# Performance work log

Measured on AMD Instinct MI355X. Metric: run time of the kernel, lower is better.

The kernel has to match this reference:

```python
import jax, jax.numpy as jnp
import numpy as np

D_IN = 1024
D_OUT = 1024

def setup_inputs() -> dict:
    key = jax.random.key(0)
    k1, k2 = jax.random.split(key)
    x = jax.random.normal(k1, (4, 2048, D_IN), dtype=jnp.float32)
    # Keras 'uniform' initializer: U(-0.05, 0.05); kernel has 4 slices, only 0..2 used
    kernel = jax.random.uniform(k2, (4, D_IN, D_OUT), dtype=jnp.float32, minval=-0.05, maxval=0.05)
    return {"x": x, "kernel": kernel}

def reference(x, kernel):
    # QKV projections: x [b, s, d] @ kernel[i] [d, e]
    WQ = jnp.einsum('bsd,de->bse', x, kernel[0])
    WK = jnp.einsum('bsd,de->bse', x, kernel[1])
    WV = jnp.einsum('bsd,de->bse', x, kernel[2])
    scale = 1.0 / jnp.sqrt(jnp.asarray(D_OUT, dtype=WQ.dtype))
    QK = jnp.einsum('bqe,bke->bqk', WQ, WK) * scale  # [b, s, s]
    A = jax.nn.softmax(QK, axis=-1)
    return jnp.einsum('bqk,bke->bqe', A, WV)  # [b, s, e]
```

## Files before the change

kernel.cpp:

```cpp
#include <hip/hip_runtime.h>
#include <hip/hip_bf16.h>
#include <cstdio>

typedef __bf16  bf16x8 __attribute__((ext_vector_type(8)));
typedef float   f32x4  __attribute__((ext_vector_type(4)));
typedef unsigned short u16;
typedef u16     u16x8  __attribute__((ext_vector_type(8)));
typedef u16     u16x4  __attribute__((ext_vector_type(4)));


__device__ __forceinline__ void gld_lds16(const void* g, void* l) {
  __builtin_amdgcn_global_load_lds(
      (const __attribute__((address_space(1))) unsigned int*)g,
      (__attribute__((address_space(3))) unsigned int*)l,
      16, 0, 0);
}

__device__ __forceinline__ u16 f2bf(float f) {
  union { float f; unsigned int u; } c{f};
  unsigned int u = c.u;
  u += 0x7fffu + ((u >> 16) & 1u);
  return (u16)(u >> 16);
}

__device__ __forceinline__ float bf2f(u16 h) {
  union { unsigned int u; float f; } c{(unsigned int)h << 16};
  return c.f;
}

enum { EPI_QKV = 0, EPI_QK = 1, EPI_PV = 2, EPI_VT = 3 };


__global__ __launch_bounds__(256) void prep_kernel(const float* __restrict__ x,
                                                   u16* __restrict__ xbf,
                                                   const float* __restrict__ w,
                                                   u16* __restrict__ wt,
                                                   float* __restrict__ rs) {
  __shared__ float tile[32][33];
  const int bid = blockIdx.x;
  if (bid < 4096) {
    const int i = (bid * 256 + threadIdx.x) * 8;
    float4 a = *(const float4*)(x + i);
    float4 b = *(const float4*)(x + i + 4);
    u16x8 r;
    r[0] = f2bf(a.x); r[1] = f2bf(a.y); r[2] = f2bf(a.z); r[3] = f2bf(a.w);
    r[4] = f2bf(b.x); r[5] = f2bf(b.y); r[6] = f2bf(b.z); r[7] = f2bf(b.w);
    *(u16x8*)(xbf + i) = r;
  } else if (bid < 7168) {
    const int b2 = bid - 4096;
    const int s = b2 >> 10, r = b2 & 1023;
    const int e0 = (r & 31) * 32, d0 = (r >> 5) * 32;
    const int tx = threadIdx.x & 31, ty = threadIdx.x >> 5;
    const float* in = w + (size_t)s * 1048576;
#pragma unroll
    for (int j = 0; j < 4; ++j)
      tile[ty + j * 8][tx] = in[(size_t)(d0 + ty + j * 8) * 1024 + e0 + tx];
    __syncthreads();
    u16* o = wt + (size_t)s * 1048576;
#pragma unroll
    for (int j = 0; j < 4; ++j)
      o[(size_t)(e0 + ty + j * 8) * 1024 + d0 + tx] = f2bf(tile[tx][ty + j * 8]);
  } else {
    const float4 z = {0.f, 0.f, 0.f, 0.f};
#pragma unroll
    for (int j = 0; j < 8; ++j)
      ((float4*)rs)[threadIdx.x + j * 256] = z;
  }
}


template <int GX, int GY, int GZ>
__device__ __forceinline__ void xcd_swz(int& bx, int& by, int& bz) {
  constexpr int NWG = GX * GY * GZ;
  static_assert(NWG % 8 == 0, "grid must be divisible by 8");
  constexpr int Q8 = NWG / 8;
  int flat = blockIdx.x + GX * (blockIdx.y + GY * blockIdx.z);
  flat = (flat & 7) * Q8 + (flat >> 3);
  bx = flat % GX;
  by = (flat / GX) % GY;
  bz = flat / (GX * GY);
}


__device__ __forceinline__ void stage_half(const u16* __restrict__ g, int ld, int k0,
                                           u16* ldsb, int w, int l) {
  const int srow = l >> 3;
  const int scol = ((l & 7) ^ (srow & 7)) * 8;
#pragma unroll
  for (int q = 0; q < 2; ++q) {
    const int r = w * 16 + q * 8;
    gld_lds16(g + (long)(r + srow) * ld + k0 + scol, (void*)(ldsb + r * 64));
  }
}

template <int EPI, int GX, int GY, int GZ>
__global__ __launch_bounds__(512, 2)
void gemm256_bt(const u16* __restrict__ A, const u16* __restrict__ B,
                void* __restrict__ Cv, int K, int lda, int ldb, int ldc,
                long sA, long sB, long sC,
                float* __restrict__ rowsum, u16* __restrict__ auxK, u16* __restrict__ auxV) {
  __shared__ __align__(16) u16 lds[65536];

  const int t = threadIdx.x;
  const int w = t >> 6, l = t & 63;
  const int wm = w >> 2, wn = w & 3;
  const int lr = l & 15, lq = l >> 4;
  const int rsw = l & 7;
  int bxs, bys, bz;
  xcd_swz<GX, GY, GZ>(bxs, bys, bz);
  const int m0 = bys * 256, n0 = bxs * 256;
  const u16* Ar = A + (long)bz * sA + (long)m0 * lda;
  const u16* Br = B + (long)bz * sB + (long)n0 * ldb;

  u16* curA = lds;
  u16* curB = lds + 16384;
  u16* nxtA = lds + 32768;
  u16* nxtB = lds + 49152;

  const int nt = K >> 6;

  f32x4 acc[8][4] = {};

  stage_half(Ar,             lda, 0, curA,        w, l);
  stage_half(Br,             ldb, 0, curB,        w, l);
  stage_half(Br + 128 * ldb, ldb, 0, curB + 8192, w, l);
  stage_half(Ar + 128 * lda, lda, 0, curA + 8192, w, l);
  asm volatile("s_waitcnt vmcnt(4)" ::: "memory");
  if (nt > 1) {
    stage_half(Ar,             lda, 64, nxtA,        w, l);
    stage_half(Br,             ldb, 64, nxtB,        w, l);
    stage_half(Br + 128 * ldb, ldb, 64, nxtB + 8192, w, l);
    asm volatile("s_waitcnt vmcnt(6)" ::: "memory");
  } else {
    asm volatile("s_waitcnt vmcnt(0)" ::: "memory");
  }
  __builtin_amdgcn_s_barrier();

  for (int tt = 0; tt < nt; ++tt) {
    const int kc = tt << 6;
    bf16x8 a0[4][2], a1[4][2], b0[2][2], b1[2][2];

#pragma unroll
    for (int mi = 0; mi < 4; ++mi)
#pragma unroll
      for (int j = 0; j < 2; ++j)
        a0[mi][j] = *(const bf16x8*)(curA + (wm * 128 + mi * 16 + lr) * 64 +
                                     (((j * 4 + lq) ^ rsw) * 8));
#pragma unroll
    for (int ni = 0; ni < 2; ++ni)
#pragma unroll
      for (int j = 0; j < 2; ++j)
        b0[ni][j] = *(const bf16x8*)(curB + (wn * 64 + ni * 16 + lr) * 64 +
                                     (((j * 4 + lq) ^ rsw) * 8));
    if (tt + 1 < nt)
      stage_half(Ar + 128 * lda, lda, kc + 64, nxtA + 8192, w, l);
    __builtin_amdgcn_s_barrier();
    asm volatile("s_waitcnt lgkmcnt(0)" ::: "memory");
    __builtin_amdgcn_sched_barrier(0);
    __builtin_amdgcn_s_setprio(1);
#pragma unroll
    for (int mi = 0; mi < 4; ++mi)
#pragma unroll
      for (int ni = 0; ni < 2; ++ni)
#pragma unroll
        for (int j = 0; j < 2; ++j)
          acc[mi][ni] = __builtin_amdgcn_mfma_f32_16x16x32_bf16(a0[mi][j], b0[ni][j], acc[mi][ni], 0, 0, 0);
    __builtin_amdgcn_s_setprio(0);
    __builtin_amdgcn_s_barrier();

#pragma unroll
    for (int ni = 0; ni < 2; ++ni)
#pragma unroll
      for (int j = 0; j < 2; ++j)
        b1[ni][j] = *(const bf16x8*)(curB + (wn * 64 + (ni + 2) * 16 + lr) * 64 +
                                     (((j * 4 + lq) ^ rsw) * 8));
    __builtin_amdgcn_s_barrier();
    asm volatile("s_waitcnt lgkmcnt(0)" ::: "memory");
    __builtin_amdgcn_sched_barrier(0);
    __builtin_amdgcn_s_setprio(1);
#pragma unroll
    for (int mi = 0; mi < 4; ++mi)
#pragma unroll
      for (int ni = 0; ni < 2; ++ni)
#pragma unroll
        for (int j = 0; j < 2; ++j)
          acc[mi][ni + 2] = __builtin_amdgcn_mfma_f32_16x16x32_bf16(a0[mi][j], b1[ni][j], acc[mi][ni + 2], 0, 0, 0);
    __builtin_amdgcn_s_setprio(0);
    __builtin_amdgcn_s_barrier();

#pragma unroll
    for (int mi = 0; mi < 4; ++mi)
#pragma unroll
      for (int j = 0; j < 2; ++j)
        a1[mi][j] = *(const bf16x8*)(curA + (wm * 128 + (mi + 4) * 16 + lr) * 64 +
                                     (((j * 4 + lq) ^ rsw) * 8));
    if (tt + 2 < nt)
      stage_half(Br, ldb, kc + 128, curB, w, l);
    __builtin_amdgcn_s_barrier();
    asm volatile("s_waitcnt lgkmcnt(0)" ::: "memory");
    __builtin_amdgcn_sched_barrier(0);
    __builtin_amdgcn_s_setprio(1);
#pragma unroll
    for (int mi = 0; mi < 4; ++mi)
#pragma unroll
      for (int ni = 0; ni < 2; ++ni)
#pragma unroll
        for (int j = 0; j < 2; ++j)
          acc[mi + 4][ni + 2] = __builtin_amdgcn_mfma_f32_16x16x32_bf16(a1[mi][j], b1[ni][j], acc[mi + 4][ni + 2], 0, 0, 0);
    __builtin_amdgcn_s_setprio(0);
    __builtin_amdgcn_s_barrier();

    if (tt + 2 < nt) {
      stage_half(Br + 128 * ldb, ldb, kc + 128, curB + 8192, w, l);
      stage_half(Ar,             lda, kc + 128, curA,        w, l);
    }
    __builtin_amdgcn_s_barrier();
    __builtin_amdgcn_sched_barrier(0);
    __builtin_amdgcn_s_setprio(1);
#pragma unroll
    for (int mi = 0; mi < 4; ++mi)
#pragma unroll
      for (int ni = 0; ni < 2; ++ni)
#pragma unroll
        for (int j = 0; j < 2; ++j)
          acc[mi + 4][ni] = __builtin_amdgcn_mfma_f32_16x16x32_bf16(a1[mi][j], b0[ni][j], acc[mi + 4][ni], 0, 0, 0);
    __builtin_amdgcn_s_setprio(0);
    if (tt + 2 < nt)      asm volatile("s_waitcnt vmcnt(6)" ::: "memory");
    else if (tt + 1 < nt) asm volatile("s_waitcnt vmcnt(0)" ::: "memory");
    __builtin_amdgcn_s_barrier();

    { u16* x_ = curA; curA = nxtA; nxtA = x_; }
    { u16* y_ = curB; curB = nxtB; nxtB = y_; }
  }

  if (EPI == EPI_QK) {
#pragma unroll
    for (int mi = 0; mi < 8; ++mi) {
#pragma unroll
      for (int i = 0; i < 4; ++i) {
        const int row = m0 + wm * 128 + mi * 16 + lq * 4 + i;
        float rs = 0.f;
#pragma unroll
        for (int ni = 0; ni < 4; ++ni) {
          const int col = n0 + wn * 64 + ni * 16 + lr;
          const u16 h = f2bf(__expf(acc[mi][ni][i] * 0.03125f));
          ((u16*)Cv)[(long)bz * sC + (long)row * ldc + col] = h;
          rs += bf2f(h);
        }
        rs += __shfl_xor(rs, 1, 64);
        rs += __shfl_xor(rs, 2, 64);
        rs += __shfl_xor(rs, 4, 64);
        rs += __shfl_xor(rs, 8, 64);
        if (lr == 0) atomicAdd(rowsum + bz * 2048 + row, rs);
      }
    }
    return;
  }

  u16* qkv_out = (n0 < 1024) ? (u16*)Cv : auxK;
  const int nl0 = n0 & 1023;
#pragma unroll
  for (int mi = 0; mi < 8; ++mi) {
#pragma unroll
    for (int i = 0; i < 4; ++i) {
      const int row = m0 + wm * 128 + mi * 16 + lq * 4 + i;
#pragma unroll
      for (int ni = 0; ni < 4; ++ni)
        qkv_out[(long)row * 1024 + nl0 + wn * 64 + ni * 16 + lr] = f2bf(acc[mi][ni][i]);
    }
  }
}


template <int EPI, int GX, int GY, int GZ>
__global__ __launch_bounds__(256)
void gemm_bt(const u16* __restrict__ A, const u16* __restrict__ B,
             void* __restrict__ Cv, int K, int lda, int ldb, int ldc,
             long sA, long sB, long sC,
             float* __restrict__ rowsum, u16* __restrict__ auxK, u16* __restrict__ auxV) {
  __shared__ __align__(16) u16 lds[128 * 128];
  u16* As = lds;
  u16* Bs = lds + 128 * 64;

  const int t = threadIdx.x;
  const int w = t >> 6, l = t & 63;
  int bxs, bys, bz;
  xcd_swz<GX, GY, GZ>(bxs, bys, bz);
  const u16* Ab = A + (long)bz * sA;
  const u16* Bb = B + (long)bz * sB;
  const int m0 = bys * 128, n0 = bxs * 128;
  const int wm = w & 1, wn = w >> 1;
  const int lr = l & 15, lq = l >> 4;
  const int srow = l >> 3;
  const int scol = ((l & 7) ^ ((l >> 3) & 7)) * 8;
  const int rsw = l & 7;

  f32x4 acc[4][4] = {};

  for (int k0 = 0; k0 < K; k0 += 64) {
    __syncthreads();
#pragma unroll
    for (int c = 0; c < 4; ++c) {
      const int rb = (w * 4 + c) * 8;
      gld_lds16(Ab + (long)(m0 + rb + srow) * lda + k0 + scol, (void*)(As + rb * 64));
      gld_lds16(Bb + (long)(n0 + rb + srow) * ldb + k0 + scol, (void*)(Bs + rb * 64));
    }
    __syncthreads();
#pragma unroll
    for (int j = 0; j < 2; ++j) {
      bf16x8 af[4], bfr[4];
#pragma unroll
      for (int i = 0; i < 4; ++i) {
        const int ch = ((j * 4 + lq) ^ rsw) * 8;
        af[i]  = *(const bf16x8*)(As + (wm * 64 + i * 16 + lr) * 64 + ch);
        bfr[i] = *(const bf16x8*)(Bs + (wn * 64 + i * 16 + lr) * 64 + ch);
      }
#pragma unroll
      for (int mi = 0; mi < 4; ++mi)
#pragma unroll
        for (int ni = 0; ni < 4; ++ni)
          acc[mi][ni] = __builtin_amdgcn_mfma_f32_16x16x32_bf16(af[mi], bfr[ni], acc[mi][ni], 0, 0, 0);
    }
  }

#pragma unroll
  for (int mi = 0; mi < 4; ++mi) {
#pragma unroll
    for (int i = 0; i < 4; ++i) {
      const int row = m0 + wm * 64 + mi * 16 + lq * 4 + i;
      float inv;
      if (EPI == EPI_PV) inv = 1.0f / rowsum[bz * 2048 + row];
      float rs = 0.f;
#pragma unroll
      for (int ni = 0; ni < 4; ++ni) {
        const float val = acc[mi][ni][i];
        const int col = n0 + wn * 64 + ni * 16 + lr;
        if (EPI == EPI_VT) {
          auxV[(long)(col >> 11) * 2097152 + (long)row * 2048 + (col & 2047)] = f2bf(val);
        } else if (EPI == EPI_QK) {
          const u16 h = f2bf(__expf(val * 0.03125f));
          ((u16*)Cv)[(long)bz * sC + (long)row * ldc + col] = h;
          rs += bf2f(h);
        } else {
          ((float*)Cv)[(long)bz * sC + (long)row * ldc + col] = val * inv;
        }
      }
      if (EPI == EPI_QK) {
        rs += __shfl_xor(rs, 1, 64);
        rs += __shfl_xor(rs, 2, 64);
        rs += __shfl_xor(rs, 4, 64);
        rs += __shfl_xor(rs, 8, 64);
        if (lr == 0) atomicAdd(rowsum + bz * 2048 + row, rs);
      }
    }
  }
}


extern "C" void kernel_launch(void* const* d_in, const int* in_sizes, int n_in,
                              void* d_out, int out_size, void* d_ws, size_t ws_size,
                              hipStream_t stream) {
  (void)in_sizes; (void)n_in; (void)out_size;
  const float* x    = (const float*)d_in[0];
  const float* kern = (const float*)d_in[1];
  float* out = (float*)d_out;
  char* ws = (char*)d_ws;
  const size_t MB = 1024 * 1024;
  u16*   xbf  = (u16*)(ws);
  u16*   WT   = (u16*)(ws + 16 * MB);
  u16*   Qc   = (u16*)(ws + 22 * MB);
  u16*   Kc   = (u16*)(ws + 38 * MB);
  u16*   VT   = (u16*)(ws + 54 * MB);
  u16*   SP   = (u16*)(ws + 70 * MB);
  float* RS   = (float*)(ws + 102 * MB);
  if (ws_size < 102 * MB + 32768)
    fprintf(stderr, "WARNING: ws_size %zu too small\n", ws_size);

  prep_kernel<<<7169, 256, 0, stream>>>(x, xbf, kern, WT, RS);
  gemm256_bt<EPI_QKV, 8, 32, 1><<<dim3(8, 32, 1), 512, 0, stream>>>(
      xbf, WT, Qc, 1024, 1024, 1024, 1024, 0, 0, 0, nullptr, Kc, nullptr);
  gemm_bt<EPI_VT, 64, 8, 1><<<dim3(64, 8, 1), 256, 0, stream>>>(
      WT + 2 * 1048576, xbf, nullptr, 1024, 1024, 1024, 2048,
      0, 0, 0, nullptr, nullptr, VT);
  gemm256_bt<EPI_QK, 8, 8, 4><<<dim3(8, 8, 4), 512, 0, stream>>>(
      Qc, Kc, SP, 1024, 1024, 1024, 2048,
      2048L * 1024, 2048L * 1024, 2048L * 2048, RS, nullptr, nullptr);
  gemm_bt<EPI_PV, 8, 16, 4><<<dim3(8, 16, 4), 256, 0, stream>>>(
      SP, VT, out, 2048, 2048, 2048, 1024,
      2048L * 2048, 1024L * 2048, 2048L * 1024, RS, nullptr, nullptr);
}
```

Before: 242.9 us.

## Restructure GEMM main loop into two-phase ping-pong with register-prefetched B fragments

Replaces the four-phase per-tile schedule, which had many barriers, with a two-phase schedule. The loop is unrolled by two over ping-pong LDS buffers via a macro. The next tile's A and B fragments are loaded into alternating register sets (bE/bO) while the current tile's MFMAs run, and the LDS buffer is refilled one tile ahead, cutting barriers per tile from eight to two. This trades more live VGPRs (two full B fragment sets) and coarser synchronization for less barrier stall. It assumes an even tile count, since the second macro call runs for tt+1 without a bound check.

```diff
diff --git a/kernel.cpp b/kernel.cpp
--- a/kernel.cpp
+++ b/kernel.cpp
@@ -93,6 +93,75 @@
   }
 }
 
+#define KT2(CA, CB, NA, NB, BC0, BC1, BN0, BN1, TT)                               \
+  do {                                                                            \
+           \
+    if ((TT) + 2 < nt) {                                                          \
+      stage_half(Br,             ldb, ((TT) + 2) << 6, lds + (CB),        w, l);  \
+      stage_half(Br + 128 * ldb, ldb, ((TT) + 2) << 6, lds + (CB) + 8192, w, l);  \
+    }                                                                             \
+    _Pragma("unroll")                                                             \
+    for (int mi = 0; mi < 4; ++mi)                                                \
+      _Pragma("unroll")                                                           \
+      for (int j = 0; j < 2; ++j)                                                 \
+        a1[mi][j] = *(const bf16x8*)(lds + (CA) +                                 \
+            (wm * 128 + (mi + 4) * 16 + lr) * 64 + (((j * 4 + lq) ^ rsw) * 8));   \
+    __builtin_amdgcn_s_setprio(1);                                                \
+    _Pragma("unroll")                                                             \
+    for (int mi = 0; mi < 4; ++mi)                                                \
+      _Pragma("unroll")                                                           \
+      for (int ni = 0; ni < 2; ++ni)                                              \
+        _Pragma("unroll")                                                         \
+        for (int j = 0; j < 2; ++j) {                                             \
+          acc[mi][ni]     = __builtin_amdgcn_mfma_f32_16x16x32_bf16(              \
+              a0[mi][j], BC0[ni][j], acc[mi][ni], 0, 0, 0);                       \
+          acc[mi][ni + 2] = __builtin_amdgcn_mfma_f32_16x16x32_bf16(              \
+              a0[mi][j], BC1[ni][j], acc[mi][ni + 2], 0, 0, 0);                   \
+        }                                                                         \
+    __builtin_amdgcn_s_setprio(0);                                                \
+    asm volatile("s_waitcnt lgkmcnt(0)" ::: "memory");                            \
+    if ((TT) + 2 < nt) asm volatile("s_waitcnt vmcnt(4)" ::: "memory");           \
+    else               asm volatile("s_waitcnt vmcnt(0)" ::: "memory");           \
+    __builtin_amdgcn_s_barrier();                                                 \
+         \
+    if ((TT) + 2 < nt) {                                                          \
+      stage_half(Ar,             lda, ((TT) + 2) << 6, lds + (CA),        w, l);  \
+      stage_half(Ar + 128 * lda, lda, ((TT) + 2) << 6, lds + (CA) + 8192, w, l);  \
+    }                                                                             \
+    if ((TT) + 1 < nt) {                                                          \
+      _Pragma("unroll")                                                           \
+      for (int mi = 0; mi < 4; ++mi)                                              \
+        _Pragma("unroll")                                                         \
+        for (int j = 0; j < 2; ++j)                                               \
+          a0[mi][j] = *(const bf16x8*)(lds + (NA) +                               \
+              (wm * 128 + mi * 16 + lr) * 64 + (((j * 4 + lq) ^ rsw) * 8));       \
+      _Pragma("unroll")                                                           \
+      for (int ni = 0; ni < 2; ++ni)                                              \
+        _Pragma("unroll")                                                         \
+        for (int j = 0; j < 2; ++j) {                                             \
+          BN0[ni][j] = *(const bf16x8*)(lds + (NB) +                              \
+              (wn * 64 + ni * 16 + lr) * 64 + (((j * 4 + lq) ^ rsw) * 8));        \
+          BN1[ni][j] = *(const bf16x8*)(lds + (NB) +                              \
+              (wn * 64 + (ni + 2) * 16 + lr) * 64 + (((j * 4 + lq) ^ rsw) * 8));  \
+        }                                                                         \
+    }                                                                             \
+    __builtin_amdgcn_s_setprio(1);                                                \
+    _Pragma("unroll")                                                             \
+    for (int mi = 0; mi < 4; ++mi)                                                \
+      _Pragma("unroll")                                                           \
+      for (int ni = 0; ni < 2; ++ni)                                              \
+        _Pragma("unroll")                                                         \
+        for (int j = 0; j < 2; ++j) {                                             \
+          acc[mi + 4][ni + 2] = __builtin_amdgcn_mfma_f32_16x16x32_bf16(          \
+              a1[mi][j], BC1[ni][j], acc[mi + 4][ni + 2], 0, 0, 0);               \
+          acc[mi + 4][ni]     = __builtin_amdgcn_mfma_f32_16x16x32_bf16(          \
+              a1[mi][j], BC0[ni][j], acc[mi + 4][ni], 0, 0, 0);                   \
+        }                                                                         \
+    __builtin_amdgcn_s_setprio(0);                                                \
+    asm volatile("s_waitcnt lgkmcnt(0)" ::: "memory");                            \
+    __builtin_amdgcn_s_barrier();                                                 \
+  } while (0)
+
 template <int EPI, int GX, int GY, int GZ>
 __global__ __launch_bounds__(512, 2)
 void gemm256_bt(const u16* __restrict__ A, const u16* __restrict__ B,
@@ -112,125 +181,48 @@
   const u16* Ar = A + (long)bz * sA + (long)m0 * lda;
   const u16* Br = B + (long)bz * sB + (long)n0 * ldb;
 
-  u16* curA = lds;
-  u16* curB = lds + 16384;
-  u16* nxtA = lds + 32768;
-  u16* nxtB = lds + 49152;
-
   const int nt = K >> 6;
 
   f32x4 acc[8][4] = {};
-
-  stage_half(Ar,             lda, 0, curA,        w, l);
-  stage_half(Br,             ldb, 0, curB,        w, l);
-  stage_half(Br + 128 * ldb, ldb, 0, curB + 8192, w, l);
-  stage_half(Ar + 128 * lda, lda, 0, curA + 8192, w, l);
-  asm volatile("s_waitcnt vmcnt(4)" ::: "memory");
+  bf16x8 a0[4][2], a1[4][2];
+  bf16x8 bE0[2][2], bE1[2][2], bO0[2][2], bO1[2][2];
+
+  stage_half(Br,             ldb, 0, lds + 16384, w, l);
+  stage_half(Br + 128 * ldb, ldb, 0, lds + 24576, w, l);
+  stage_half(Ar,             lda, 0, lds,         w, l);
+  stage_half(Ar + 128 * lda, lda, 0, lds + 8192,  w, l);
   if (nt > 1) {
-    stage_half(Ar,             lda, 64, nxtA,        w, l);
-    stage_half(Br,             ldb, 64, nxtB,        w, l);
-    stage_half(Br + 128 * ldb, ldb, 64, nxtB + 8192, w, l);
-    asm volatile("s_waitcnt vmcnt(6)" ::: "memory");
+    stage_half(Br,             ldb, 64, lds + 49152, w, l);
+    stage_half(Br + 128 * ldb, ldb, 64, lds + 57344, w, l);
+    stage_half(Ar,             lda, 64, lds + 32768, w, l);
+    stage_half(Ar + 128 * lda, lda, 64, lds + 40960, w, l);
+    asm volatile("s_waitcnt vmcnt(8)" ::: "memory");
   } else {
     asm volatile("s_waitcnt vmcnt(0)" ::: "memory");
   }
   __builtin_amdgcn_s_barrier();
 
-  for (int tt = 0; tt < nt; ++tt) {
-    const int kc = tt << 6;
-    bf16x8 a0[4][2], a1[4][2], b0[2][2], b1[2][2];
-
-#pragma unroll
-    for (int mi = 0; mi < 4; ++mi)
-#pragma unroll
-      for (int j = 0; j < 2; ++j)
-        a0[mi][j] = *(const bf16x8*)(curA + (wm * 128 + mi * 16 + lr) * 64 +
-                                     (((j * 4 + lq) ^ rsw) * 8));
-#pragma unroll
-    for (int ni = 0; ni < 2; ++ni)
-#pragma unroll
-      for (int j = 0; j < 2; ++j)
-        b0[ni][j] = *(const bf16x8*)(curB + (wn * 64 + ni * 16 + lr) * 64 +
-                                     (((j * 4 + lq) ^ rsw) * 8));
-    if (tt + 1 < nt)
-      stage_half(Ar + 128 * lda, lda, kc + 64, nxtA + 8192, w, l);
-    __builtin_amdgcn_s_barrier();
-    asm volatile("s_waitcnt lgkmcnt(0)" ::: "memory");
-    __builtin_amdgcn_sched_barrier(0);
-    __builtin_amdgcn_s_setprio(1);
-#pragma unroll
-    for (int mi = 0; mi < 4; ++mi)
-#pragma unroll
-      for (int ni = 0; ni < 2; ++ni)
-#pragma unroll
-        for (int j = 0; j < 2; ++j)
-          acc[mi][ni] = __builtin_amdgcn_mfma_f32_16x16x32_bf16(a0[mi][j], b0[ni][j], acc[mi][ni], 0, 0, 0);
-    __builtin_amdgcn_s_setprio(0);
-    __builtin_amdgcn_s_barrier();
-
-#pragma unroll
-    for (int ni = 0; ni < 2; ++ni)
-#pragma unroll
-      for (int j = 0; j < 2; ++j)
-        b1[ni][j] = *(const bf16x8*)(curB + (wn * 64 + (ni + 2) * 16 + lr) * 64 +
-                                     (((j * 4 + lq) ^ rsw) * 8));
-    __builtin_amdgcn_s_barrier();
-    asm volatile("s_waitcnt lgkmcnt(0)" ::: "memory");
-    __builtin_amdgcn_sched_barrier(0);
-    __builtin_amdgcn_s_setprio(1);
-#pragma unroll
-    for (int mi = 0; mi < 4; ++mi)
-#pragma unroll
-      for (int ni = 0; ni < 2; ++ni)
-#pragma unroll
-        for (int j = 0; j < 2; ++j)
-          acc[mi][ni + 2] = __builtin_amdgcn_mfma_f32_16x16x32_bf16(a0[mi][j], b1[ni][j], acc[mi][ni + 2], 0, 0, 0);
-    __builtin_amdgcn_s_setprio(0);
-    __builtin_amdgcn_s_barrier();
-
-#pragma unroll
-    for (int mi = 0; mi < 4; ++mi)
-#pragma unroll
-      for (int j = 0; j < 2; ++j)
-        a1[mi][j] = *(const bf16x8*)(curA + (wm * 128 + (mi + 4) * 16 + lr) * 64 +
-                                     (((j * 4 + lq) ^ rsw) * 8));
-    if (tt + 2 < nt)
-      stage_half(Br, ldb, kc + 128, curB, w, l);
-    __builtin_amdgcn_s_barrier();
-    asm volatile("s_waitcnt lgkmcnt(0)" ::: "memory");
-    __builtin_amdgcn_sched_barrier(0);
-    __builtin_amdgcn_s_setprio(1);
-#pragma unroll
-    for (int mi = 0; mi < 4; ++mi)
-#pragma unroll
-      for (int ni = 0; ni < 2; ++ni)
-#pragma unroll
-        for (int j = 0; j < 2; ++j)
-          acc[mi + 4][ni + 2] = __builtin_amdgcn_mfma_f32_16x16x32_bf16(a1[mi][j], b1[ni][j], acc[mi + 4][ni + 2], 0, 0, 0);
-    __builtin_amdgcn_s_setprio(0);
-    __builtin_amdgcn_s_barrier();
-
-    if (tt + 2 < nt) {
-      stage_half(Br + 128 * ldb, ldb, kc + 128, curB + 8192, w, l);
-      stage_half(Ar,             lda, kc + 128, curA,        w, l);
-    }
-    __builtin_amdgcn_s_barrier();
-    __builtin_amdgcn_sched_barrier(0);
-    __builtin_amdgcn_s_setprio(1);
-#pragma unroll
-    for (int mi = 0; mi < 4; ++mi)
-#pragma unroll
-      for (int ni = 0; ni < 2; ++ni)
-#pragma unroll
-        for (int j = 0; j < 2; ++j)
-          acc[mi + 4][ni] = __builtin_amdgcn_mfma_f32_16x16x32_bf16(a1[mi][j], b0[ni][j], acc[mi + 4][ni], 0, 0, 0);
-    __builtin_amdgcn_s_setprio(0);
-    if (tt + 2 < nt)      asm volatile("s_waitcnt vmcnt(6)" ::: "memory");
-    else if (tt + 1 < nt) asm volatile("s_waitcnt vmcnt(0)" ::: "memory");
-    __builtin_amdgcn_s_barrier();
-
-    { u16* x_ = curA; curA = nxtA; nxtA = x_; }
-    { u16* y_ = curB; curB = nxtB; nxtB = y_; }
+#pragma unroll
+  for (int mi = 0; mi < 4; ++mi)
+#pragma unroll
+    for (int j = 0; j < 2; ++j)
+      a0[mi][j] = *(const bf16x8*)(lds + (wm * 128 + mi * 16 + lr) * 64 +
+                                   (((j * 4 + lq) ^ rsw) * 8));
+#pragma unroll
+  for (int ni = 0; ni < 2; ++ni)
+#pragma unroll
+    for (int j = 0; j < 2; ++j) {
+      bE0[ni][j] = *(const bf16x8*)(lds + 16384 + (wn * 64 + ni * 16 + lr) * 64 +
+                                    (((j * 4 + lq) ^ rsw) * 8));
+      bE1[ni][j] = *(const bf16x8*)(lds + 16384 + (wn * 64 + (ni + 2) * 16 + lr) * 64 +
+                                    (((j * 4 + lq) ^ rsw) * 8));
+    }
+  asm volatile("s_waitcnt lgkmcnt(0)" ::: "memory");
+  __builtin_amdgcn_s_barrier();
+
+  for (int tt = 0; tt < nt; tt += 2) {
+    KT2(0,     16384, 32768, 49152, bE0, bE1, bO0, bO1, tt);
+    KT2(32768, 49152, 0,     16384, bO0, bO1, bE0, bE1, tt + 1);
   }
 
   if (EPI == EPI_QK) {
```

After: 395.7 us. 62.9% more time.
